# Performance work log

Measured on AMD Instinct MI355X. Metric: run time of the kernel, lower is better.

Reference implementation:

```python
import jax, jax.numpy as jnp
import numpy as np

ALPHA = 0.2  # leaky relu slope
NEG = -9e15

N, NFEAT, NHID, NHEADS = 4096, 1024, 64, 8
EMB = NHID * NHEADS  # 512


def setup_inputs() -> dict:
    key = jax.random.key(0)
    ks = jax.random.split(key, 16)
    x = jax.random.normal(ks[0], (N, NFEAT), dtype=jnp.float32)
    adj = (jax.random.uniform(ks[1], (N, N)) < 0.01).astype(jnp.float32)
    adj = jnp.maximum(adj, jnp.eye(N, dtype=jnp.float32))
    s = 0.05
    W = jax.random.normal(ks[2], (NHEADS, NFEAT, NHID), dtype=jnp.float32) * s
    a1 = jax.random.normal(ks[3], (NHEADS, NHID), dtype=jnp.float32) * s
    a2 = jax.random.normal(ks[4], (NHEADS, NHID), dtype=jnp.float32) * s
    # decoder: 512 -> 256 -> 256 -> 512 -> 1024 (PyTorch Linear convention: y = x @ W.T + b)
    W1 = jax.random.normal(ks[5], (EMB // 2, EMB), dtype=jnp.float32) * s
    b1 = jnp.zeros((EMB // 2,), dtype=jnp.float32)
    W2 = jax.random.normal(ks[6], (NFEAT // 4, EMB // 2), dtype=jnp.float32) * s
    b2 = jnp.zeros((NFEAT // 4,), dtype=jnp.float32)
    W3 = jax.random.normal(ks[7], (NFEAT // 2, NFEAT // 4), dtype=jnp.float32) * s
    b3 = jnp.zeros((NFEAT // 2,), dtype=jnp.float32)
    W4 = jax.random.normal(ks[8], (NFEAT, NFEAT // 2), dtype=jnp.float32) * s
    b4 = jnp.zeros((NFEAT,), dtype=jnp.float32)
    return {"x": x, "adj": adj, "W": W, "a1": a1, "a2": a2,
            "W1": W1, "b1": b1, "W2": W2, "b2": b2,
            "W3": W3, "b3": b3, "W4": W4, "b4": b4}


def reference(x, adj, W, a1, a2, W1, b1, W2, b2, W3, b3, W4, b4):
    # --- encoder: multi-head GAT (dropout=0) ---
    Wh = jnp.einsum('nf,hfd->hnd', x, W)              # [H, N, nhid]
    e_src = jnp.einsum('hnd,hd->hn', Wh, a1)          # [H, N]
    e_dst = jnp.einsum('hnd,hd->hn', Wh, a2)          # [H, N]
    e = jax.nn.leaky_relu(e_src[:, :, None] + e_dst[:, None, :], ALPHA)  # [H, N, N]
    e = jnp.where(adj[None] > 0, e, NEG)
    att = jax.nn.softmax(e, axis=-1)
    h = jnp.einsum('hnm,hmd->hnd', att, Wh)           # [H, N, nhid]
    h = jax.nn.elu(h)                                 # concat=True -> elu per layer
    enc = jnp.transpose(h, (1, 0, 2)).reshape(x.shape[0], -1)  # [N, H*nhid]
    # --- decoder: 4-layer MLP ---
    out = jax.nn.relu(enc @ W1.T + b1)
    out = jax.nn.relu(out @ W2.T + b2)
    out = jax.nn.relu(out @ W3.T + b3)
    out = out @ W4.T + b4
    return out
```

## Files before the change

kernel.cpp:

```cpp
#include <hip/hip_runtime.h>
#include <hip/hip_bf16.h>
#include <math.h>

#define NNODES 4096
#define NFEAT_ 1024
#define NHID_  64
#define NHEADS_ 8
#define EMB_   512
#define MAXD   256
constexpr float ALPHA_ = 0.2f;

typedef __attribute__((ext_vector_type(8))) short bf16x8;
typedef __attribute__((ext_vector_type(4))) float f32x4;

__device__ inline unsigned short f2b(float f) {
    __hip_bfloat16 b = __float2bfloat16(f);
    return *(unsigned short*)&b;
}

template<int BN, bool OUTBF, int ACT>
__global__ __launch_bounds__(256) void gemm_bt(
    const unsigned short* __restrict__ A, const unsigned short* __restrict__ B,
    const float* __restrict__ bias, void* __restrict__ Cv,
    int M, int N, int K)
{
    constexpr int BM = 128, BK = 32;
    constexpr int NJ = BN / 32;
    constexpr int WN = BN / 2;
    __shared__ __align__(16) unsigned short As[BM * BK];
    __shared__ __align__(16) unsigned short Bs[BN * BK];

    const int tid  = threadIdx.x;
    const int wid  = tid >> 6, lane = tid & 63;
    const int wr   = wid >> 1, wc = wid & 1;
    const int m0   = blockIdx.y * BM, n0 = blockIdx.x * BN;
    const int frow = lane & 15, fk = (lane >> 4) * 8;

    f32x4 acc[4][NJ] = {};

    for (int k0 = 0; k0 < K; k0 += BK) {
        const uint4* ga = (const uint4*)(A + (long)m0 * K + k0);
        #pragma unroll
        for (int i = 0; i < 2; ++i) {
            const int c = i * 256 + tid;
            ((uint4*)As)[c] = ga[(long)(c >> 2) * (K >> 3) + (c & 3)];
        }
        const uint4* gb = (const uint4*)(B + (long)n0 * K + k0);
        #pragma unroll
        for (int i = 0; i < BN / 64; ++i) {
            const int c = i * 256 + tid;
            ((uint4*)Bs)[c] = gb[(long)(c >> 2) * (K >> 3) + (c & 3)];
        }
        __syncthreads();

        bf16x8 af[4], bfr[NJ];
        #pragma unroll
        for (int i = 0; i < 4; ++i)
            af[i] = *(const bf16x8*)&As[(wr * 64 + i * 16 + frow) * BK + fk];
        #pragma unroll
        for (int j = 0; j < NJ; ++j)
            bfr[j] = *(const bf16x8*)&Bs[(wc * WN + j * 16 + frow) * BK + fk];
        #pragma unroll
        for (int i = 0; i < 4; ++i)
            #pragma unroll
            for (int j = 0; j < NJ; ++j)
                acc[i][j] = __builtin_amdgcn_mfma_f32_16x16x32_bf16(
                    af[i], bfr[j], acc[i][j], 0, 0, 0);
        __syncthreads();
    }

    const int crow0 = m0 + wr * 64 + (lane >> 4) * 4;
    const int ccol0 = n0 + wc * WN + (lane & 15);
    #pragma unroll
    for (int i = 0; i < 4; ++i)
        #pragma unroll
        for (int j = 0; j < NJ; ++j)
            #pragma unroll
            for (int r = 0; r < 4; ++r) {
                const int row = crow0 + i * 16 + r;
                const int col = ccol0 + j * 16;
                float v = acc[i][j][r];
                if (bias) v += bias[col];
                if (ACT == 1) v = v > 0.f ? v : 0.f;
                if (OUTBF) ((unsigned short*)Cv)[(long)row * N + col] = f2b(v);
                else       ((float*)Cv)[(long)row * N + col] = v;
            }
}

__global__ __launch_bounds__(256) void prep(
    const float* __restrict__ x,  const float* __restrict__ W,
    const float* __restrict__ W1, const float* __restrict__ W2,
    const float* __restrict__ W3, const float* __restrict__ W4,
    unsigned short* __restrict__ xb,  unsigned short* __restrict__ WcT,
    unsigned short* __restrict__ W1b, unsigned short* __restrict__ W2b,
    unsigned short* __restrict__ W3b, unsigned short* __restrict__ W4b)
{
    const int np = gridDim.x * 256;
    const int t  = blockIdx.x * 256 + threadIdx.x;

    for (int i = t; i < (NNODES * NFEAT_) / 4; i += np) {
        const float4 v = ((const float4*)x)[i];
        ushort4 o; o.x = f2b(v.x); o.y = f2b(v.y); o.z = f2b(v.z); o.w = f2b(v.w);
        ((ushort4*)xb)[i] = o;
    }
    for (int i = t; i < EMB_ * NFEAT_; i += np) {
        const int nrow = i >> 10, k = i & 1023;
        const int h = nrow >> 6, d = nrow & 63;
        WcT[i] = f2b(W[((long)h * NFEAT_ + k) * NHID_ + d]);
    }
    for (int i = t; i < (256 * 512) / 4; i += np) {
        const float4 v = ((const float4*)W1)[i];
        ushort4 o; o.x = f2b(v.x); o.y = f2b(v.y); o.z = f2b(v.z); o.w = f2b(v.w);
        ((ushort4*)W1b)[i] = o;
    }
    for (int i = t; i < (256 * 256) / 4; i += np) {
        const float4 v = ((const float4*)W2)[i];
        ushort4 o; o.x = f2b(v.x); o.y = f2b(v.y); o.z = f2b(v.z); o.w = f2b(v.w);
        ((ushort4*)W2b)[i] = o;
    }
    for (int i = t; i < (512 * 256) / 4; i += np) {
        const float4 v = ((const float4*)W3)[i];
        ushort4 o; o.x = f2b(v.x); o.y = f2b(v.y); o.z = f2b(v.z); o.w = f2b(v.w);
        ((ushort4*)W3b)[i] = o;
    }
    for (int i = t; i < (1024 * 512) / 4; i += np) {
        const float4 v = ((const float4*)W4)[i];
        ushort4 o; o.x = f2b(v.x); o.y = f2b(v.y); o.z = f2b(v.z); o.w = f2b(v.w);
        ((ushort4*)W4b)[i] = o;
    }
}

__global__ __launch_bounds__(256) void attn_scores(
    const float* __restrict__ Whc, const float* __restrict__ a1,
    const float* __restrict__ a2, float* __restrict__ esrc,
    float* __restrict__ edst)
{
    const int wave = (blockIdx.x * 256 + threadIdx.x) >> 6;
    const int lane = threadIdx.x & 63;
    const int h = wave >> 12, n = wave & 4095;
    const float w = Whc[(long)n * EMB_ + h * NHID_ + lane];
    float s1 = w * a1[h * NHID_ + lane];
    float s2 = w * a2[h * NHID_ + lane];
    #pragma unroll
    for (int off = 32; off; off >>= 1) {
        s1 += __shfl_xor(s1, off);
        s2 += __shfl_xor(s2, off);
    }
    if (lane == 0) {
        esrc[h * NNODES + n] = s1;
        edst[h * NNODES + n] = s2;
    }
}

__global__ __launch_bounds__(256) void build_nbr(
    const float* __restrict__ adj, int* __restrict__ cnt,
    int* __restrict__ nbr)
{
    __shared__ int lcnt;
    const int n = blockIdx.x;
    if (threadIdx.x == 0) lcnt = 0;
    __syncthreads();
    for (int m = threadIdx.x; m < NNODES; m += 256) {
        if (adj[(long)n * NNODES + m] != 0.f) {
            const int p = atomicAdd(&lcnt, 1);
            if (p < MAXD) nbr[n * MAXD + p] = m;
        }
    }
    __syncthreads();
    if (threadIdx.x == 0) cnt[n] = lcnt < MAXD ? lcnt : MAXD;
}

__global__ __launch_bounds__(256) void attn_agg(
    const float* __restrict__ Whc, const float* __restrict__ esrc,
    const float* __restrict__ edst, const int* __restrict__ cnt,
    const int* __restrict__ nbr, unsigned short* __restrict__ enc)
{
    __shared__ float pLds[4][MAXD];
    __shared__ int   mLds[4][MAXD];
    const int w = threadIdx.x >> 6, lane = threadIdx.x & 63;
    const int pair = blockIdx.x * 4 + w;
    const int h = pair >> 12, n = pair & 4095;

    const int deg = min(cnt[n], MAXD);
    const int* lst = nbr + n * MAXD;
    const float es = esrc[h * NNODES + n];

    float mymax = -3.4e38f;
    for (int j = lane; j < deg; j += 64) {
        const int m = lst[j];
        float ev = es + edst[h * NNODES + m];
        ev = ev > 0.f ? ev : ALPHA_ * ev;
        pLds[w][j] = ev;
        mLds[w][j] = m;
        mymax = fmaxf(mymax, ev);
    }
    #pragma unroll
    for (int off = 32; off; off >>= 1) mymax = fmaxf(mymax, __shfl_xor(mymax, off));

    float mysum = 0.f;
    for (int j = lane; j < deg; j += 64) {
        const float p = expf(pLds[w][j] - mymax);
        pLds[w][j] = p;
        mysum += p;
    }
    #pragma unroll
    for (int off = 32; off; off >>= 1) mysum += __shfl_xor(mysum, off);

    __syncthreads();

    float acc = 0.f;
    for (int j = 0; j < deg; ++j)
        acc = fmaf(pLds[w][j], Whc[(long)mLds[w][j] * EMB_ + h * NHID_ + lane], acc);

    float hv = acc / mysum;
    hv = hv > 0.f ? hv : expm1f(hv);
    enc[(long)n * EMB_ + h * NHID_ + lane] = f2b(hv);
}

extern "C" void kernel_launch(void* const* d_in, const int* in_sizes, int n_in,
                              void* d_out, int out_size, void* d_ws, size_t ws_size,
                              hipStream_t stream)
{
    const float* x   = (const float*)d_in[0];
    const float* adj = (const float*)d_in[1];
    const float* W   = (const float*)d_in[2];
    const float* a1  = (const float*)d_in[3];
    const float* a2  = (const float*)d_in[4];
    const float* W1  = (const float*)d_in[5];
    const float* b1  = (const float*)d_in[6];
    const float* W2  = (const float*)d_in[7];
    const float* b2  = (const float*)d_in[8];
    const float* W3  = (const float*)d_in[9];
    const float* b3  = (const float*)d_in[10];
    const float* W4  = (const float*)d_in[11];
    const float* b4  = (const float*)d_in[12];
    float* out = (float*)d_out;

    float* Whc = (float*)d_ws;
    float* es  = Whc + 2097152;
    float* ed  = es  + 32768;
    unsigned short* enc = (unsigned short*)(ed + 32768);
    unsigned short* WcT = enc + 2097152;
    unsigned short* W1b = WcT + 524288;
    unsigned short* W2b = W1b + 131072;
    unsigned short* W3b = W2b + 65536;
    unsigned short* W4b = W3b + 131072;
    int* cnt = (int*)(W4b + 524288);
    int* nbr = cnt + 4096;
    unsigned short* xb  = (unsigned short*)(nbr + 1048576);
    unsigned short* dd1 = xb;
    unsigned short* dd2 = dd1 + 1048576;
    unsigned short* dd3 = dd2 + 1048576;

    prep<<<dim3(256), 256, 0, stream>>>(x, W, W1, W2, W3, W4,
                                        xb, WcT, W1b, W2b, W3b, W4b);

    gemm_bt<64, false, 0><<<dim3(8, 32), 256, 0, stream>>>(
        xb, WcT, nullptr, Whc, NNODES, EMB_, NFEAT_);

    attn_scores<<<dim3(8192), 256, 0, stream>>>(Whc, a1, a2, es, ed);

    build_nbr<<<dim3(NNODES), 256, 0, stream>>>(adj, cnt, nbr);

    attn_agg<<<dim3(8192), 256, 0, stream>>>(Whc, es, ed, cnt, nbr, enc);

    gemm_bt<64, true, 1><<<dim3(4, 32), 256, 0, stream>>>(enc, W1b, b1, dd1, NNODES, 256, 512);
    gemm_bt<64, true, 1><<<dim3(4, 32), 256, 0, stream>>>(dd1, W2b, b2, dd2, NNODES, 256, 256);
    gemm_bt<64, true, 1><<<dim3(8, 32), 256, 0, stream>>>(dd2, W3b, b3, dd3, NNODES, 512, 256);
    gemm_bt<128, false, 0><<<dim3(8, 32), 256, 0, stream>>>(dd3, W4b, b4, out, NNODES, 1024, 512);
}
```

Before: 271.3 us.

## Fuse prep with neighbor build, use direct-to-LDS loads and bf16 gather

Merges weight/input conversion and adjacency-to-neighbor-list construction into one launch, with float4 adjacency reads and a shared-memory tiled transpose for the GAT weight. The GEMM now stages tiles with global_load_lds direct-to-LDS copies. The first GEMM also writes a bf16 copy of Wh, so the attention aggregation gathers half-size rows. The 256-wide decoder layers use a narrower BN=32 tile to launch more blocks. The bf16 gather loses some precision in the aggregation, and the fused kernel mixes heterogeneous block roles.

```diff
diff --git a/kernel.cpp b/kernel.cpp
--- a/kernel.cpp
+++ b/kernel.cpp
@@ -12,44 +12,66 @@
 
 typedef __attribute__((ext_vector_type(8))) short bf16x8;
 typedef __attribute__((ext_vector_type(4))) float f32x4;
-
-__device__ inline unsigned short f2b(float f) {
+typedef unsigned int u32;
+typedef unsigned short u16;
+
+__device__ inline u16 f2b(float f) {
     __hip_bfloat16 b = __float2bfloat16(f);
-    return *(unsigned short*)&b;
-}
-
-template<int BN, bool OUTBF, int ACT>
+    return *(u16*)&b;
+}
+__device__ inline float b2f(u16 u) {
+    return __uint_as_float(((u32)u) << 16);
+}
+
+__device__ inline void cp16(const void* g, void* l) {
+    __builtin_amdgcn_global_load_lds(
+        (const __attribute__((address_space(1))) u32*)g,
+        (__attribute__((address_space(3))) u32*)l, 16, 0, 0);
+}
+
+template<int BN, int OUTM, int ACT>
 __global__ __launch_bounds__(256) void gemm_bt(
-    const unsigned short* __restrict__ A, const unsigned short* __restrict__ B,
+    const u16* __restrict__ A, const u16* __restrict__ B,
     const float* __restrict__ bias, void* __restrict__ Cv,
-    int M, int N, int K)
+    u16* __restrict__ Cb, int M, int N, int K)
 {
     constexpr int BM = 128, BK = 32;
-    constexpr int NJ = BN / 32;
     constexpr int WN = BN / 2;
-    __shared__ __align__(16) unsigned short As[BM * BK];
-    __shared__ __align__(16) unsigned short Bs[BN * BK];
+    constexpr int NJ = WN / 16;
+    constexpr int BCH = BN / 16;
+    __shared__ __align__(16) u16 As[BM * BK];
+    __shared__ __align__(16) u16 Bs[BN * BK];
 
     const int tid  = threadIdx.x;
     const int wid  = tid >> 6, lane = tid & 63;
     const int wr   = wid >> 1, wc = wid & 1;
     const int m0   = blockIdx.y * BM, n0 = blockIdx.x * BN;
     const int frow = lane & 15, fk = (lane >> 4) * 8;
+    const int lr   = lane >> 2, lc = (lane & 3) * 8;
 
     f32x4 acc[4][NJ] = {};
 
     for (int k0 = 0; k0 < K; k0 += BK) {
-        const uint4* ga = (const uint4*)(A + (long)m0 * K + k0);
-        #pragma unroll
-        for (int i = 0; i < 2; ++i) {
-            const int c = i * 256 + tid;
-            ((uint4*)As)[c] = ga[(long)(c >> 2) * (K >> 3) + (c & 3)];
-        }
-        const uint4* gb = (const uint4*)(B + (long)n0 * K + k0);
-        #pragma unroll
-        for (int i = 0; i < BN / 64; ++i) {
-            const int c = i * 256 + tid;
-            ((uint4*)Bs)[c] = gb[(long)(c >> 2) * (K >> 3) + (c & 3)];
+        {
+            const u16* gA = A + (long)m0 * K + k0;
+            int c = wid;
+            cp16(gA + (long)(c * 16 + lr) * K + lc, &As[c * 512]);
+            c = wid + 4;
+            cp16(gA + (long)(c * 16 + lr) * K + lc, &As[c * 512]);
+        }
+        {
+            const u16* gB = B + (long)n0 * K + k0;
+            if (BCH >= 4) {
+                int c = wid;
+                cp16(gB + (long)(c * 16 + lr) * K + lc, &Bs[c * 512]);
+                if (BCH == 8) {
+                    c = wid + 4;
+                    cp16(gB + (long)(c * 16 + lr) * K + lc, &Bs[c * 512]);
+                }
+            } else if (wid < BCH) {
+                const int c = wid;
+                cp16(gB + (long)(c * 16 + lr) * K + lc, &Bs[c * 512]);
+            }
         }
         __syncthreads();
 
@@ -82,51 +104,86 @@
                 float v = acc[i][j][r];
                 if (bias) v += bias[col];
                 if (ACT == 1) v = v > 0.f ? v : 0.f;
-                if (OUTBF) ((unsigned short*)Cv)[(long)row * N + col] = f2b(v);
-                else       ((float*)Cv)[(long)row * N + col] = v;
+                if (OUTM == 1) ((u16*)Cv)[(long)row * N + col] = f2b(v);
+                else           ((float*)Cv)[(long)row * N + col] = v;
+                if (OUTM == 2) Cb[(long)row * N + col] = f2b(v);
             }
 }
 
-__global__ __launch_bounds__(256) void prep(
-    const float* __restrict__ x,  const float* __restrict__ W,
-    const float* __restrict__ W1, const float* __restrict__ W2,
-    const float* __restrict__ W3, const float* __restrict__ W4,
-    unsigned short* __restrict__ xb,  unsigned short* __restrict__ WcT,
-    unsigned short* __restrict__ W1b, unsigned short* __restrict__ W2b,
-    unsigned short* __restrict__ W3b, unsigned short* __restrict__ W4b)
-{
-    const int np = gridDim.x * 256;
-    const int t  = blockIdx.x * 256 + threadIdx.x;
-
-    for (int i = t; i < (NNODES * NFEAT_) / 4; i += np) {
-        const float4 v = ((const float4*)x)[i];
-        ushort4 o; o.x = f2b(v.x); o.y = f2b(v.y); o.z = f2b(v.z); o.w = f2b(v.w);
-        ((ushort4*)xb)[i] = o;
-    }
-    for (int i = t; i < EMB_ * NFEAT_; i += np) {
-        const int nrow = i >> 10, k = i & 1023;
-        const int h = nrow >> 6, d = nrow & 63;
-        WcT[i] = f2b(W[((long)h * NFEAT_ + k) * NHID_ + d]);
-    }
-    for (int i = t; i < (256 * 512) / 4; i += np) {
-        const float4 v = ((const float4*)W1)[i];
-        ushort4 o; o.x = f2b(v.x); o.y = f2b(v.y); o.z = f2b(v.z); o.w = f2b(v.w);
-        ((ushort4*)W1b)[i] = o;
-    }
-    for (int i = t; i < (256 * 256) / 4; i += np) {
-        const float4 v = ((const float4*)W2)[i];
-        ushort4 o; o.x = f2b(v.x); o.y = f2b(v.y); o.z = f2b(v.z); o.w = f2b(v.w);
-        ((ushort4*)W2b)[i] = o;
-    }
-    for (int i = t; i < (512 * 256) / 4; i += np) {
-        const float4 v = ((const float4*)W3)[i];
-        ushort4 o; o.x = f2b(v.x); o.y = f2b(v.y); o.z = f2b(v.z); o.w = f2b(v.w);
-        ((ushort4*)W3b)[i] = o;
-    }
-    for (int i = t; i < (1024 * 512) / 4; i += np) {
-        const float4 v = ((const float4*)W4)[i];
-        ushort4 o; o.x = f2b(v.x); o.y = f2b(v.y); o.z = f2b(v.z); o.w = f2b(v.w);
-        ((ushort4*)W4b)[i] = o;
+__global__ __launch_bounds__(256) void prep_nbr(
+    const float* __restrict__ x,   const float* __restrict__ adj,
+    const float* __restrict__ W,
+    const float* __restrict__ W1,  const float* __restrict__ W2,
+    const float* __restrict__ W3,  const float* __restrict__ W4,
+    u16* __restrict__ xb,  u16* __restrict__ WcT,
+    u16* __restrict__ W1b, u16* __restrict__ W2b,
+    u16* __restrict__ W3b, u16* __restrict__ W4b,
+    int* __restrict__ cnt, int* __restrict__ nbr)
+{
+    const int b = blockIdx.x, tid = threadIdx.x;
+
+    if (b < NNODES) {
+        __shared__ int lcnt;
+        if (tid == 0) lcnt = 0;
+        __syncthreads();
+        const float4* arow = (const float4*)(adj + (long)b * NNODES);
+        for (int m4 = tid; m4 < NNODES / 4; m4 += 256) {
+            const float4 v = arow[m4];
+            if (v.x != 0.f) { const int p = atomicAdd(&lcnt, 1); if (p < MAXD) nbr[b * MAXD + p] = m4 * 4; }
+            if (v.y != 0.f) { const int p = atomicAdd(&lcnt, 1); if (p < MAXD) nbr[b * MAXD + p] = m4 * 4 + 1; }
+            if (v.z != 0.f) { const int p = atomicAdd(&lcnt, 1); if (p < MAXD) nbr[b * MAXD + p] = m4 * 4 + 2; }
+            if (v.w != 0.f) { const int p = atomicAdd(&lcnt, 1); if (p < MAXD) nbr[b * MAXD + p] = m4 * 4 + 3; }
+        }
+        __syncthreads();
+        if (tid == 0) cnt[b] = lcnt < MAXD ? lcnt : MAXD;
+    } else if (b < NNODES + 128) {
+        __shared__ float tile[64][65];
+        const int tb = b - NNODES;
+        const int h = tb >> 4, k0 = (tb & 15) * 64;
+        #pragma unroll
+        for (int p = 0; p < 4; ++p) {
+            const int kr = p * 16 + (tid >> 4), d = (tid & 15) * 4;
+            const float4 v = *(const float4*)&W[((long)h * NFEAT_ + k0 + kr) * NHID_ + d];
+            tile[kr][d] = v.x; tile[kr][d + 1] = v.y;
+            tile[kr][d + 2] = v.z; tile[kr][d + 3] = v.w;
+        }
+        __syncthreads();
+        #pragma unroll
+        for (int p = 0; p < 4; ++p) {
+            const int d = p * 16 + (tid >> 4), k = (tid & 15) * 4;
+            ushort4 o;
+            o.x = f2b(tile[k][d]);     o.y = f2b(tile[k + 1][d]);
+            o.z = f2b(tile[k + 2][d]); o.w = f2b(tile[k + 3][d]);
+            *(ushort4*)&WcT[((long)h * 64 + d) * NFEAT_ + k0 + k] = o;
+        }
+    } else {
+        const int np = 256 * 256;
+        const int t = (b - NNODES - 128) * 256 + tid;
+        for (int i = t; i < (NNODES * NFEAT_) / 4; i += np) {
+            const float4 v = ((const float4*)x)[i];
+            ushort4 o; o.x = f2b(v.x); o.y = f2b(v.y); o.z = f2b(v.z); o.w = f2b(v.w);
+            ((ushort4*)xb)[i] = o;
+        }
+        for (int i = t; i < (256 * 512) / 4; i += np) {
+            const float4 v = ((const float4*)W1)[i];
+            ushort4 o; o.x = f2b(v.x); o.y = f2b(v.y); o.z = f2b(v.z); o.w = f2b(v.w);
+            ((ushort4*)W1b)[i] = o;
+        }
+        for (int i = t; i < (256 * 256) / 4; i += np) {
+            const float4 v = ((const float4*)W2)[i];
+            ushort4 o; o.x = f2b(v.x); o.y = f2b(v.y); o.z = f2b(v.z); o.w = f2b(v.w);
+            ((ushort4*)W2b)[i] = o;
+        }
+        for (int i = t; i < (512 * 256) / 4; i += np) {
+            const float4 v = ((const float4*)W3)[i];
+            ushort4 o; o.x = f2b(v.x); o.y = f2b(v.y); o.z = f2b(v.z); o.w = f2b(v.w);
+            ((ushort4*)W3b)[i] = o;
+        }
+        for (int i = t; i < (1024 * 512) / 4; i += np) {
+            const float4 v = ((const float4*)W4)[i];
+            ushort4 o; o.x = f2b(v.x); o.y = f2b(v.y); o.z = f2b(v.z); o.w = f2b(v.w);
+            ((ushort4*)W4b)[i] = o;
+        }
     }
 }
 
@@ -152,28 +209,10 @@
     }
 }
 
-__global__ __launch_bounds__(256) void build_nbr(
-    const float* __restrict__ adj, int* __restrict__ cnt,
-    int* __restrict__ nbr)
-{
-    __shared__ int lcnt;
-    const int n = blockIdx.x;
-    if (threadIdx.x == 0) lcnt = 0;
-    __syncthreads();
-    for (int m = threadIdx.x; m < NNODES; m += 256) {
-        if (adj[(long)n * NNODES + m] != 0.f) {
-            const int p = atomicAdd(&lcnt, 1);
-            if (p < MAXD) nbr[n * MAXD + p] = m;
-        }
-    }
-    __syncthreads();
-    if (threadIdx.x == 0) cnt[n] = lcnt < MAXD ? lcnt : MAXD;
-}
-
 __global__ __launch_bounds__(256) void attn_agg(
-    const float* __restrict__ Whc, const float* __restrict__ esrc,
+    const u16* __restrict__ Whb, const float* __restrict__ esrc,
     const float* __restrict__ edst, const int* __restrict__ cnt,
-    const int* __restrict__ nbr, unsigned short* __restrict__ enc)
+    const int* __restrict__ nbr, u16* __restrict__ enc)
 {
     __shared__ float pLds[4][MAXD];
     __shared__ int   mLds[4][MAXD];
@@ -209,8 +248,10 @@
     __syncthreads();
 
     float acc = 0.f;
+    const u16* base = Whb + (long)h * NHID_ + lane;
+    #pragma unroll 2
     for (int j = 0; j < deg; ++j)
-        acc = fmaf(pLds[w][j], Whc[(long)mLds[w][j] * EMB_ + h * NHID_ + lane], acc);
+        acc = fmaf(pLds[w][j], b2f(base[(long)mLds[w][j] * EMB_]), acc);
 
     float hv = acc / mysum;
     hv = hv > 0.f ? hv : expm1f(hv);
@@ -239,33 +280,32 @@
     float* Whc = (float*)d_ws;
     float* es  = Whc + 2097152;
     float* ed  = es  + 32768;
-    unsigned short* enc = (unsigned short*)(ed + 32768);
-    unsigned short* WcT = enc + 2097152;
-    unsigned short* W1b = WcT + 524288;
-    unsigned short* W2b = W1b + 131072;
-    unsigned short* W3b = W2b + 65536;
-    unsigned short* W4b = W3b + 131072;
+    u16* Whb = (u16*)(ed + 32768);
+    u16* enc = Whb + 2097152;
+    u16* WcT = enc + 2097152;
+    u16* W1b = WcT + 524288;
+    u16* W2b = W1b + 131072;
+    u16* W3b = W2b + 65536;
+    u16* W4b = W3b + 131072;
     int* cnt = (int*)(W4b + 524288);
     int* nbr = cnt + 4096;
-    unsigned short* xb  = (unsigned short*)(nbr + 1048576);
-    unsigned short* dd1 = xb;
-    unsigned short* dd2 = dd1 + 1048576;
-    unsigned short* dd3 = dd2 + 1048576;
-
-    prep<<<dim3(256), 256, 0, stream>>>(x, W, W1, W2, W3, W4,
-                                        xb, WcT, W1b, W2b, W3b, W4b);
-
-    gemm_bt<64, false, 0><<<dim3(8, 32), 256, 0, stream>>>(
-        xb, WcT, nullptr, Whc, NNODES, EMB_, NFEAT_);
+    u16* xb  = (u16*)(nbr + 1048576);
+    u16* dd1 = xb;
+    u16* dd2 = dd1 + 1048576;
+    u16* dd3 = dd2 + 1048576;
+
+    prep_nbr<<<dim3(NNODES + 128 + 256), 256, 0, stream>>>(
+        x, adj, W, W1, W2, W3, W4, xb, WcT, W1b, W2b, W3b, W4b, cnt, nbr);
+
+    gemm_bt<64, 2, 0><<<dim3(8, 32), 256, 0, stream>>>(
+        xb, WcT, nullptr, Whc, Whb, NNODES, EMB_, NFEAT_);
 
     attn_scores<<<dim3(8192), 256, 0, stream>>>(Whc, a1, a2, es, ed);
 
-    build_nbr<<<dim3(NNODES), 256, 0, stream>>>(adj, cnt, nbr);
-
-    attn_agg<<<dim3(8192), 256, 0, stream>>>(Whc, es, ed, cnt, nbr, enc);
-
-    gemm_bt<64, true, 1><<<dim3(4, 32), 256, 0, stream>>>(enc, W1b, b1, dd1, NNODES, 256, 512);
-    gemm_bt<64, true, 1><<<dim3(4, 32), 256, 0, stream>>>(dd1, W2b, b2, dd2, NNODES, 256, 256);
-    gemm_bt<64, true, 1><<<dim3(8, 32), 256, 0, stream>>>(dd2, W3b, b3, dd3, NNODES, 512, 256);
-    gemm_bt<128, false, 0><<<dim3(8, 32), 256, 0, stream>>>(dd3, W4b, b4, out, NNODES, 1024, 512);
-}
+    attn_agg<<<dim3(8192), 256, 0, stream>>>(Whb, es, ed, cnt, nbr, enc);
+
+    gemm_bt<32, 1, 1><<<dim3(8, 32), 256, 0, stream>>>(enc, W1b, b1, dd1, nullptr, NNODES, 256, 512);
+    gemm_bt<32, 1, 1><<<dim3(8, 32), 256, 0, stream>>>(dd1, W2b, b2, dd2, nullptr, NNODES, 256, 256);
+    gemm_bt<64, 1, 1><<<dim3(8, 32), 256, 0, stream>>>(dd2, W3b, b3, dd3, nullptr, NNODES, 512, 256);
+    gemm_bt<128, 0, 0><<<dim3(8, 32), 256, 0, stream>>>(dd3, W4b, b4, out, nullptr, NNODES, 1024, 512);
+}
```

After: 266.8 us. No clear change (-1.7%).
